# Kernel optimization log

Hardware: AMD Instinct MI355X
Metric: run time of the kernel (lower is better)

## Reference

```python
import jax, jax.numpy as jnp
import numpy as np

K = 20
EPS = 1e-5
NEG_SLOPE = 0.2


def _knn(x):
    # x: (B, C, N) -> idx of K nearest (largest negative sq dist): (B, N, K)
    inner = -2.0 * jnp.einsum('bcn,bcm->bnm', x, x)
    xx = jnp.sum(x * x, axis=1)  # (B, N)
    pd = -xx[:, :, None] - inner - xx[:, None, :]
    return jax.lax.top_k(pd, K)[1]


def _graph_feature(x):
    # x: (B, C, N) -> (B, 2C, N, K) edge features cat(nbr - center, center)
    idx = _knn(x)                              # (B, N, K)
    xt = jnp.swapaxes(x, 1, 2)                 # (B, N, C)
    nbr = jax.vmap(lambda f, i: f[i])(xt, idx)  # (B, N, K, C)
    center = xt[:, :, None, :]
    feat = jnp.concatenate([nbr - center, jnp.broadcast_to(center, nbr.shape)], axis=-1)
    return jnp.transpose(feat, (0, 3, 1, 2))


def _bn(x, g, b, m, v):
    # inference-mode batchnorm over channel axis 1
    shp = [1] * x.ndim
    shp[1] = -1
    scale = (g / jnp.sqrt(v + EPS)).reshape(shp)
    return (x - m.reshape(shp)) * scale + b.reshape(shp)


def _lrelu(x):
    return jnp.where(x >= 0, x, NEG_SLOPE * x)


def setup_inputs() -> dict:
    key = jax.random.key(0)
    ks = jax.random.split(key, 16)
    d = {
        'x': jax.random.normal(ks[0], (4, 2, 4096), jnp.float32),
        'W1': jax.random.normal(ks[1], (64, 4), jnp.float32),
        'g1': jax.random.uniform(ks[2], (64,), jnp.float32),
        'b1': jax.random.normal(ks[3], (64,), jnp.float32),
        'm1': jnp.zeros((64,), jnp.float32),
        'v1': jnp.ones((64,), jnp.float32),
        'W2': jax.random.normal(ks[4], (64, 128), jnp.float32),
        'g2': jax.random.uniform(ks[5], (64,), jnp.float32),
        'b2': jax.random.normal(ks[6], (64,), jnp.float32),
        'm2': jnp.zeros((64,), jnp.float32),
        'v2': jnp.ones((64,), jnp.float32),
        'W5': jax.random.normal(ks[7], (128, 128), jnp.float32),
        'g5': jax.random.uniform(ks[8], (128,), jnp.float32),
        'b5': jax.random.normal(ks[9], (128,), jnp.float32),
        'm5': jnp.zeros((128,), jnp.float32),
        'v5': jnp.ones((128,), jnp.float32),
        'W6': jax.random.normal(ks[10], (256, 256), jnp.float32),
        'g6': jax.random.uniform(ks[11], (256,), jnp.float32),
        'b6': jax.random.normal(ks[12], (256,), jnp.float32),
        'm6': jnp.zeros((256,), jnp.float32),
        'v6': jnp.ones((256,), jnp.float32),
        'W9': jax.random.normal(ks[13], (1, 256), jnp.float32),
    }
    return d


def reference(x, W1, g1, b1, m1, v1, W2, g2, b2, m2, v2,
              W5, g5, b5, m5, v5, W6, g6, b6, m6, v6, W9):
    B, _, N = x.shape
    # EdgeConv 1
    f = _graph_feature(x)                                     # (B, 4, N, K)
    h = _lrelu(_bn(jnp.einsum('bcnk,oc->bonk', f, W1), g1, b1, m1, v1))
    x1 = jnp.max(h, axis=-1)                                  # (B, 64, N)
    # EdgeConv 2 (graph rebuilt in feature space)
    f = _graph_feature(x1)                                    # (B, 128, N, K)
    h = _lrelu(_bn(jnp.einsum('bcnk,oc->bonk', f, W2), g2, b2, m2, v2))
    x2 = jnp.max(h, axis=-1)                                  # (B, 64, N)
    xc = jnp.concatenate([x1, x2], axis=1)                    # (B, 128, N)
    # conv5 (1x1 conv1d) + global max pool
    h5 = _lrelu(_bn(jnp.einsum('bcn,oc->bon', xc, W5), g5, b5, m5, v5))  # (B, 128, N)
    gmax = jnp.max(h5, axis=-1)                               # (B, 128)
    rep = jnp.broadcast_to(gmax[:, :, None], (B, gmax.shape[1], N))
    cat = jnp.concatenate([rep, xc], axis=1)                  # (B, 256, N)
    # conv6 (dropout is identity in eval) then conv9
    h6 = _lrelu(_bn(jnp.einsum('bcn,oc->bon', cat, W6), g6, b6, m6, v6))
    out = jnp.einsum('bcn,oc->bon', h6, W9)                   # (B, 1, N)
    return out.reshape(B, N)
```

## Files before the change

kernel.cpp:

```cpp
#include <hip/hip_runtime.h>
#include <math.h>

#define NEGINF (-INFINITY)
constexpr int Np = 4096;
constexpr int Kn = 20;
constexpr float EPSf = 1e-5f;
constexpr float SLOPE = 0.2f;

typedef __bf16 bf16x8 __attribute__((ext_vector_type(8)));
typedef float f32x4 __attribute__((ext_vector_type(4)));
typedef unsigned long long ull;
typedef unsigned int u32;
typedef unsigned short u16;

__global__ __launch_bounds__(512, 2) void k1_knn1_edge1(
    const float* __restrict__ x, const float* __restrict__ W1,
    const float* __restrict__ g1, const float* __restrict__ b1,
    const float* __restrict__ m1, const float* __restrict__ v1,
    float* __restrict__ x1, __bf16* __restrict__ x1h, __bf16* __restrict__ x1l,
    float* __restrict__ xx2)
{
  __shared__ u32 smem32[16000];
  float* pk1  = (float*)smem32;
  u16*   pi1  = (u16*)((char*)smem32 + 32768);
  u32*   thrK = (u32*)((char*)smem32 + 49152);
  u32*   ku   = smem32;
  u16*   ki   = (u16*)((char*)smem32 + 40960);
  u16*   midx = (u16*)((char*)smem32 + 61440);
  float* nbr  = (float*)smem32;

  const int b = blockIdx.y;
  const int n0 = blockIdx.x * 64;
  const int tid = threadIdx.x;
  const int w = tid >> 6, L = tid & 63;
  const float* __restrict__ xr = x + (size_t)b*2*Np;
  const float* __restrict__ yr = xr + Np;

  const int n = n0 + L;
  const float px = xr[n], py = yr[n];

  if (tid < 64) thrK[tid] = 0xFFFFFFFFu;
  __syncthreads();

  ull kv[20];
#pragma unroll
  for (int s = 0; s < 20; ++s) kv[s] = 0ull;
  u32 u_cut = 0xFFFFFFFFu;
  int cnt = 0;

  auto flushK = [&]() {
#pragma unroll 1
    for (int f0 = 0; f0 < 16; f0 += 4) {
      if (__all(f0 >= cnt)) break;
      float fv[4]; u32 ji[4];
#pragma unroll
      for (int u = 0; u < 4; ++u) {
        fv[u] = pk1[(f0+u)*512 + tid];
        ji[u] = pi1[(f0+u)*512 + tid];
      }
#pragma unroll
      for (int u = 0; u < 4; ++u) {
        int f = f0 + u;
        ull key = (((ull)(~__float_as_uint(fv[u]))) << 32) | (u32)~ji[u];
        if (f < cnt && key > kv[19]) {
          ull ck = key;
#pragma unroll
          for (int s = 0; s < 20; ++s) {
            bool sw = ck > kv[s];
            ull tv = kv[s];
            kv[s] = sw ? ck : kv[s];
            ck = sw ? tv : ck;
          }
        }
      }
    }
    cnt = 0;
    u32 uc = ~(u32)(kv[19] >> 32);
    atomicMin(&thrK[L], uc);
    u_cut = thrK[L];
  };

  const int base = w * 512;
#pragma unroll 1
  for (int j0 = base; j0 < base + 512; j0 += 16) {
    {
      u32 hs = thrK[L];
      u_cut = hs < u_cut ? hs : u_cut;
    }
#pragma unroll
    for (int c = 0; c < 4; ++c) {
      float4 xv = *reinterpret_cast<const float4*>(xr + j0 + c*4);
      float4 yv = *reinterpret_cast<const float4*>(yr + j0 + c*4);
      const float xs[4] = {xv.x, xv.y, xv.z, xv.w};
      const float ys[4] = {yv.x, yv.y, yv.z, yv.w};
#pragma unroll
      for (int r = 0; r < 4; ++r) {
        float dx = xs[r] - px, dy = ys[r] - py;
        float s = dx*dx + dy*dy;
        u32 ub = __float_as_uint(s);
        if (ub <= u_cut) {
          pk1[cnt*512 + tid] = s;
          pi1[cnt*512 + tid] = (u16)(j0 + c*4 + r);
          ++cnt;
        }
      }
      if (__any(cnt >= 13)) flushK();
    }
  }
  flushK();

  __syncthreads();
#pragma unroll
  for (int k = 0; k < Kn; ++k) {
    ku[((size_t)w*64 + L)*20 + k] = (u32)(kv[k] >> 32);
    ki[((size_t)w*64 + L)*20 + k] = (u16)~(u32)kv[k];
  }
  __syncthreads();

  if (tid < 64) {
    const int p = tid;
    u32 hk_[8]; u16 hj_[8]; int pc[8];
#pragma unroll
    for (int q = 0; q < 8; ++q) {
      size_t bi = ((size_t)q*64 + p)*20;
      hk_[q] = ku[bi]; hj_[q] = ki[bi]; pc[q] = 0;
    }
    for (int k = 0; k < Kn; ++k) {
      u32 bk = hk_[0]; u16 bj = hj_[0]; int sel = 0;
#pragma unroll
      for (int q = 1; q < 8; ++q) {
        bool better = (hk_[q] > bk) || (hk_[q] == bk && hj_[q] < bj);
        if (better) { bk = hk_[q]; bj = hj_[q]; sel = q; }
      }
      midx[p*20 + k] = bj;
      int np_ = ++pc[sel];
      size_t bi = ((size_t)sel*64 + p)*20;
      hk_[sel] = (np_ < 20) ? ku[bi + np_] : 0u;
      hj_[sel] = (np_ < 20) ? ki[bi + np_] : (u16)0xFFFF;
    }
  }
  __syncthreads();

  for (int i = tid; i < 64*Kn; i += 512) {
    int j = midx[i];
    nbr[i*2]     = xr[j];
    nbr[i*2 + 1] = yr[j];
  }
  __syncthreads();

  const int o = L;
  const float4 w1v = reinterpret_cast<const float4*>(W1)[o];
  const float sc = g1[o] / sqrtf(v1[o] + EPSf);
  const float mo = m1[o], bo = b1[o];

  for (int pi = 0; pi < 8; ++pi) {
    const int p = w*8 + pi;
    const int np = n0 + p;
    const float cx0 = xr[np], cx1 = yr[np];
    const float cterm = (w1v.z - w1v.x)*cx0 + (w1v.w - w1v.y)*cx1;
    float xm = NEGINF;
#pragma unroll
    for (int k = 0; k < Kn; ++k) {
      float2 nv = *reinterpret_cast<const float2*>(&nbr[(p*20 + k)*2]);
      float vv = w1v.x*nv.x + w1v.y*nv.y + cterm;
      float h = (vv - mo)*sc + bo;
      h = h >= 0.f ? h : SLOPE*h;
      xm = fmaxf(xm, h);
    }
    x1[(b*64 + o)*Np + np] = xm;
    __bf16 hb = (__bf16)xm;
    __bf16 lb = (__bf16)(xm - (float)hb);
    size_t tbase = ((size_t)b*Np + np)*64 + o;
    x1h[tbase] = hb;
    x1l[tbase] = lb;
    float s = xm*xm;
#pragma unroll
    for (int off = 1; off < 64; off <<= 1) s += __shfl_xor(s, off);
    if (L == 0) xx2[b*Np + np] = s;
  }
}

__global__ __launch_bounds__(256, 2) void k2_knn2(
    const __bf16* __restrict__ xh, const __bf16* __restrict__ xl,
    const float* __restrict__ xx2, int* __restrict__ idx2)
{
  __shared__ ull smem[5120];
  float* sxx = (float*)smem;
  float* pk  = (float*)((char*)smem + 16384);
  u16*   pi  = (u16*)((char*)smem + 31744);
  u32*   thr = (u32*)((char*)smem + 39424);

  const int b = blockIdx.y;
  const int n0 = blockIdx.x * 16;
  const int tid = threadIdx.x;
  const int w = tid >> 6, L = tid & 63;
  const int L15 = L & 15, quad = L >> 4;

  for (int j = tid*4; j < Np; j += 1024)
    *reinterpret_cast<float4*>(&sxx[j]) = *reinterpret_cast<const float4*>(&xx2[(size_t)b*Np + j]);
  if (tid < 16) thr[tid] = 0u;

  const __bf16* Rh = xh + ((size_t)b*Np + n0)*64;
  const __bf16* Rl = xl + ((size_t)b*Np + n0)*64;
  bf16x8 rh0 = *reinterpret_cast<const bf16x8*>(Rh + L15*64 +  0 + quad*8);
  bf16x8 rh1 = *reinterpret_cast<const bf16x8*>(Rh + L15*64 + 32 + quad*8);
  bf16x8 rl0 = *reinterpret_cast<const bf16x8*>(Rl + L15*64 +  0 + quad*8);
  bf16x8 rl1 = *reinterpret_cast<const bf16x8*>(Rl + L15*64 + 32 + quad*8);

  const __bf16* Cbh = xh + (size_t)b*Np*64;
  const __bf16* Cbl = xl + (size_t)b*Np*64;

  ull kv[20];
#pragma unroll
  for (int s = 0; s < 20; ++s) kv[s] = 0ull;
  float fthresh = NEGINF;
  int cnt = 0;

  __syncthreads();

  auto flush = [&]() {
#pragma unroll 1
    for (int f0 = 0; f0 < 15; f0 += 4) {
      if (__all(f0 >= cnt)) break;
      float fv[4]; u32 ji[4];
#pragma unroll
      for (int u = 0; u < 4; ++u) {
        fv[u] = pk[(f0+u)*256 + tid];
        ji[u] = pi[(f0+u)*256 + tid];
      }
#pragma unroll
      for (int u = 0; u < 4; ++u) {
        int f = f0 + u;
        u32 uu = __float_as_uint(fv[u]);
        u32 hk = uu ^ ((u32)((int)uu >> 31) | 0x80000000u);
        ull key = (((ull)hk) << 32) | (u32)~ji[u];
        if (f < cnt && key > kv[19]) {
          ull ck = key;
#pragma unroll
          for (int s = 0; s < 20; ++s) {
            bool sw = ck > kv[s];
            ull tv = kv[s];
            kv[s] = sw ? ck : kv[s];
            ck = sw ? tv : ck;
          }
        }
      }
    }
    cnt = 0;
    ull t = kv[19];
    ull t2 = __shfl_xor(t, 16); t = t2 > t ? t2 : t;
    t2 = __shfl_xor(t, 32);     t = t2 > t ? t2 : t;
    if (t != 0ull && quad == 0) atomicMax(&thr[L15], (u32)(t >> 32));
    u32 hs = thr[L15];
    if (hs != 0u) {
      u32 u = (hs >> 31) ? (hs ^ 0x80000000u) : ~hs;
      fthresh = fmaxf(fthresh, __uint_as_float(u));
    }
  };

#pragma unroll 1
  for (int t = 0; t < 16; ++t) {
    {
      u32 hs = thr[L15];
      if (hs != 0u) {
        u32 u = (hs >> 31) ? (hs ^ 0x80000000u) : ~hs;
        fthresh = fmaxf(fthresh, __uint_as_float(u));
      }
    }
    const int tt = w + t*4;
    const int colbase = tt * 64;
    const __bf16* ph = Cbh + (size_t)colbase*64;
    const __bf16* pl = Cbl + (size_t)colbase*64;
    bf16x8 AH[4][2], AL[4][2];
#pragma unroll
    for (int s = 0; s < 4; ++s) {
      AH[s][0] = *reinterpret_cast<const bf16x8*>(ph + (s*16 + L15)*64 +  0 + quad*8);
      AH[s][1] = *reinterpret_cast<const bf16x8*>(ph + (s*16 + L15)*64 + 32 + quad*8);
      AL[s][0] = *reinterpret_cast<const bf16x8*>(pl + (s*16 + L15)*64 +  0 + quad*8);
      AL[s][1] = *reinterpret_cast<const bf16x8*>(pl + (s*16 + L15)*64 + 32 + quad*8);
    }

    f32x4 acc[4];
#pragma unroll
    for (int s = 0; s < 4; ++s) {
      acc[s] = (f32x4){0.f, 0.f, 0.f, 0.f};
      acc[s] = __builtin_amdgcn_mfma_f32_16x16x32_bf16(AH[s][0], rh0, acc[s], 0, 0, 0);
      acc[s] = __builtin_amdgcn_mfma_f32_16x16x32_bf16(AH[s][1], rh1, acc[s], 0, 0, 0);
      acc[s] = __builtin_amdgcn_mfma_f32_16x16x32_bf16(AH[s][0], rl0, acc[s], 0, 0, 0);
      acc[s] = __builtin_amdgcn_mfma_f32_16x16x32_bf16(AH[s][1], rl1, acc[s], 0, 0, 0);
      acc[s] = __builtin_amdgcn_mfma_f32_16x16x32_bf16(AL[s][0], rh0, acc[s], 0, 0, 0);
      acc[s] = __builtin_amdgcn_mfma_f32_16x16x32_bf16(AL[s][1], rh1, acc[s], 0, 0, 0);
    }

#pragma unroll
    for (int s = 0; s < 4; ++s) {
      float4 xv = *reinterpret_cast<const float4*>(&sxx[colbase + s*16 + quad*4]);
      const float xvr[4] = {xv.x, xv.y, xv.z, xv.w};
#pragma unroll
      for (int r = 0; r < 4; ++r) {
        float e = 2.0f*acc[s][r] - xvr[r];
        if (e >= fthresh) {
          pk[cnt*256 + tid] = e;
          pi[cnt*256 + tid] = (u16)(colbase + s*16 + quad*4 + r);
          ++cnt;
        }
      }
      if (__any(cnt >= 12)) flush();
    }
  }
  flush();

  __syncthreads();
#pragma unroll
  for (int k = 0; k < Kn; ++k) smem[((size_t)w*64 + L)*20 + k] = kv[k];
  __syncthreads();

  if (tid < 16) {
    const int r = tid;
    ull h[16]; int pc[16];
#pragma unroll
    for (int i = 0; i < 16; ++i) {
      h[i] = smem[((size_t)(i>>2)*64 + (i&3)*16 + r)*20];
      pc[i] = 0;
    }
    size_t obase = ((size_t)b*Np + n0 + r)*Kn;
    for (int k = 0; k < Kn; ++k) {
      ull best = h[0]; int sel = 0;
#pragma unroll
      for (int i = 1; i < 16; ++i) if (h[i] > best) { best = h[i]; sel = i; }
      idx2[obase + k] = (int)~(u32)best;
      int np_ = ++pc[sel];
      h[sel] = (np_ < 20) ? smem[((size_t)(sel>>2)*64 + (sel&3)*16 + r)*20 + np_] : 0ull;
    }
  }
}

__global__ __launch_bounds__(256) void kY(
    const __bf16* __restrict__ xh, const __bf16* __restrict__ xl,
    const float* __restrict__ W2,
    const float* __restrict__ g2, const float* __restrict__ b2,
    const float* __restrict__ m2, const float* __restrict__ v2,
    float* __restrict__ Za, float* __restrict__ Cn)
{
  __shared__ float w2t[128*66];
  const int b = blockIdx.y;
  const int n0 = blockIdx.x * 16;
  const int tid = threadIdx.x;
  const int w = tid >> 6, L = tid & 63;

  for (int i = tid; i < 8192; i += 256) {
    int o = i >> 7, c = i & 127;
    w2t[c*66 + o] = W2[i];
  }
  __syncthreads();

  const float sc = g2[L] / sqrtf(v2[L] + EPSf);
  const float cc = b2[L] - m2[L]*sc;

  for (int pi = 0; pi < 4; ++pi) {
    const int n = n0 + w*4 + pi;
    const size_t base = ((size_t)b*Np + n)*64;
    const float xv = (float)xh[base + L] + (float)xl[base + L];
    float ya = 0.f, yb = 0.f;
#pragma unroll
    for (int c = 0; c < 64; ++c) {
      float xc = __shfl(xv, c);
      ya += w2t[c*66 + L] * xc;
      yb += w2t[(64 + c)*66 + L] * xc;
    }
    float za = sc * ya;
    Za[base + L] = za;
    Cn[base + L] = sc * yb + cc - za;
  }
}

__global__ __launch_bounds__(256, 2) void k3_gather(
    const float* __restrict__ Za, const float* __restrict__ Cn,
    const int* __restrict__ idx2, float* __restrict__ x2)
{
  const int b = blockIdx.y;
  const int tid = threadIdx.x;
  const int w = tid >> 6, L = tid & 63;
  const int n = blockIdx.x*4 + w;

  const int* ip = idx2 + ((size_t)b*Np + n)*Kn;
  int jreg = (L < Kn) ? ip[L] : 0;
  const float c = Cn[((size_t)b*Np + n)*64 + L];
  float xm = NEGINF;
#pragma unroll
  for (int k = 0; k < Kn; ++k) {
    int j = __shfl(jreg, k);
    float hh = Za[((size_t)b*Np + j)*64 + L] + c;
    hh = hh >= 0.f ? hh : SLOPE*hh;
    xm = fmaxf(xm, hh);
  }
  x2[(b*64 + L)*Np + n] = xm;
}

__global__ __launch_bounds__(512) void k4_conv5max(
    const float* __restrict__ x1, const float* __restrict__ x2,
    const float* __restrict__ W5,
    const float* __restrict__ g5, const float* __restrict__ b5,
    const float* __restrict__ m5, const float* __restrict__ v5,
    float* __restrict__ partials)
{
  const int b = blockIdx.y;
  const int nb = blockIdx.x >> 1, half = blockIdx.x & 1;
  const int tid = threadIdx.x;
  const int p = tid & 63;
  const int g = __builtin_amdgcn_readfirstlane(tid >> 6);
  const int n = nb*64 + p;
  float xcr[128];
#pragma unroll
  for (int c = 0; c < 64; ++c) {
    xcr[c]    = x1[(b*64 + c)*Np + n];
    xcr[64+c] = x2[(b*64 + c)*Np + n];
  }
  for (int oi = 0; oi < 8; ++oi) {
    const int o = half*64 + g*8 + oi;
    const float* wr = W5 + o*128;
    float dot = 0.f;
#pragma unroll
    for (int c = 0; c < 128; c += 4) {
      float4 wv = *reinterpret_cast<const float4*>(wr + c);
      dot += wv.x*xcr[c] + wv.y*xcr[c+1] + wv.z*xcr[c+2] + wv.w*xcr[c+3];
    }
    float hv = (dot - m5[o])*(g5[o]/sqrtf(v5[o]+EPSf)) + b5[o];
    hv = hv >= 0.f ? hv : SLOPE*hv;
#pragma unroll
    for (int off = 1; off < 64; off <<= 1) hv = fmaxf(hv, __shfl_xor(hv, off));
    if (p == 0) partials[(b*128 + o)*64 + nb] = hv;
  }
}

__global__ __launch_bounds__(256) void k5_reduce_t6(
    const float* __restrict__ partials, const float* __restrict__ W6,
    float* __restrict__ t6)
{
  __shared__ float sg[128];
  const int b = blockIdx.x;
  const int tid = threadIdx.x;
  if (tid < 128) {
    const float4* pr = reinterpret_cast<const float4*>(partials + ((size_t)b*128 + tid)*64);
    float m = NEGINF;
#pragma unroll
    for (int w = 0; w < 16; ++w) {
      float4 v = pr[w];
      m = fmaxf(m, fmaxf(fmaxf(v.x, v.y), fmaxf(v.z, v.w)));
    }
    sg[tid] = m;
  }
  __syncthreads();
  float a = 0.f;
#pragma unroll
  for (int c = 0; c < 128; c += 4) {
    float4 wv = *reinterpret_cast<const float4*>(W6 + tid*256 + c);
    a += wv.x*sg[c] + wv.y*sg[c+1] + wv.z*sg[c+2] + wv.w*sg[c+3];
  }
  t6[b*256 + tid] = a;
}

__global__ __launch_bounds__(512) void k6_conv6_out(
    const float* __restrict__ x1, const float* __restrict__ x2,
    const float* __restrict__ W6, const float* __restrict__ t6,
    const float* __restrict__ g6, const float* __restrict__ b6,
    const float* __restrict__ m6, const float* __restrict__ v6,
    const float* __restrict__ W9,
    float* __restrict__ out)
{
  __shared__ float red[8][64];
  const int b = blockIdx.y, nb = blockIdx.x;
  const int tid = threadIdx.x;
  const int p = tid & 63;
  const int g = __builtin_amdgcn_readfirstlane(tid >> 6);
  const int n = nb*64 + p;
  float xcr[128];
#pragma unroll
  for (int c = 0; c < 64; ++c) {
    xcr[c]    = x1[(b*64 + c)*Np + n];
    xcr[64+c] = x2[(b*64 + c)*Np + n];
  }
  float oacc = 0.f;
  for (int oi = 0; oi < 32; ++oi) {
    const int o = g*32 + oi;
    const float* wr = W6 + o*256 + 128;
    float dot = t6[b*256 + o];
#pragma unroll
    for (int c = 0; c < 128; c += 4) {
      float4 wv = *reinterpret_cast<const float4*>(wr + c);
      dot += wv.x*xcr[c] + wv.y*xcr[c+1] + wv.z*xcr[c+2] + wv.w*xcr[c+3];
    }
    float hv = (dot - m6[o])*(g6[o]/sqrtf(v6[o]+EPSf)) + b6[o];
    hv = hv >= 0.f ? hv : SLOPE*hv;
    oacc += W9[o]*hv;
  }
  red[g][p] = oacc;
  __syncthreads();
  if (tid < 64) {
    float s = 0.f;
#pragma unroll
    for (int q = 0; q < 8; ++q) s += red[q][tid];
    out[b*Np + nb*64 + tid] = s;
  }
}

extern "C" void kernel_launch(void* const* d_in, const int* in_sizes, int n_in,
                              void* d_out, int out_size, void* d_ws, size_t ws_size,
                              hipStream_t stream) {
  const float* x  = (const float*)d_in[0];
  const float* W1 = (const float*)d_in[1];
  const float* g1 = (const float*)d_in[2];
  const float* b1 = (const float*)d_in[3];
  const float* m1 = (const float*)d_in[4];
  const float* v1 = (const float*)d_in[5];
  const float* W2 = (const float*)d_in[6];
  const float* g2 = (const float*)d_in[7];
  const float* b2 = (const float*)d_in[8];
  const float* m2 = (const float*)d_in[9];
  const float* v2 = (const float*)d_in[10];
  const float* W5 = (const float*)d_in[11];
  const float* g5 = (const float*)d_in[12];
  const float* b5 = (const float*)d_in[13];
  const float* m5 = (const float*)d_in[14];
  const float* v5 = (const float*)d_in[15];
  const float* W6 = (const float*)d_in[16];
  const float* g6 = (const float*)d_in[17];
  const float* b6 = (const float*)d_in[18];
  const float* m6 = (const float*)d_in[19];
  const float* v6 = (const float*)d_in[20];
  const float* W9 = (const float*)d_in[21];
  float* out = (float*)d_out;

  float* F = (float*)d_ws;
  float*  x1    = F;
  float*  xx2   = F + 1048576;
  __bf16* x1h   = (__bf16*)(F + 1064960);
  __bf16* x1l   = (__bf16*)(F + 1589248);
  float*  x2    = F + 2113536;
  int*    idx2  = (int*)(F + 3162112);
  float*  t6    = F + 3489792;
  float*  parts = F + 3490816;
  float*  Za    = F + 3523584;
  float*  Cn    = F + 4572160;

  k1_knn1_edge1<<<dim3(64,4), 512, 0, stream>>>(x, W1, g1, b1, m1, v1, x1, x1h, x1l, xx2);
  k2_knn2<<<dim3(256,4), 256, 0, stream>>>(x1h, x1l, xx2, idx2);
  kY<<<dim3(256,4), 256, 0, stream>>>(x1h, x1l, W2, g2, b2, m2, v2, Za, Cn);
  k3_gather<<<dim3(1024,4), 256, 0, stream>>>(Za, Cn, idx2, x2);
  k4_conv5max<<<dim3(128,4), 512, 0, stream>>>(x1, x2, W5, g5, b5, m5, v5, parts);
  k5_reduce_t6<<<4, 256, 0, stream>>>(parts, W6, t6);
  k6_conv6_out<<<dim3(64,4), 512, 0, stream>>>(x1, x2, W6, t6, g6, b6, m6, v6, W9, out);
}
```

Measured before the change: 524.9 us.

## Fuse W2 projection into knn1 kernel and split conv6 output channels across blocks

The per-point W2 projection (Za/Cn) is moved from a separate kernel into the tail of the first EdgeConv kernel. It reuses the freshly computed x1 values held in registers, which avoids a launch and a reread of x1h/x1l. Separately, conv6 is split across twice as many blocks, each covering half the output channels, with partial results combined by atomicAdd into an output zeroed by a memset. This adds LDS use and tail work to k1, which runs only 256 blocks, plus an extra memset and atomics. It also changes the float summation order, and the fused path now reads exact fp32 x1 instead of the bf16 hi+lo reconstruction.

```diff
diff --git a/kernel.cpp b/kernel.cpp
--- a/kernel.cpp
+++ b/kernel.cpp
@@ -17,8 +17,11 @@
     const float* __restrict__ x, const float* __restrict__ W1,
     const float* __restrict__ g1, const float* __restrict__ b1,
     const float* __restrict__ m1, const float* __restrict__ v1,
+    const float* __restrict__ W2,
+    const float* __restrict__ g2, const float* __restrict__ b2,
+    const float* __restrict__ m2, const float* __restrict__ v2,
     float* __restrict__ x1, __bf16* __restrict__ x1h, __bf16* __restrict__ x1l,
-    float* __restrict__ xx2)
+    float* __restrict__ xx2, float* __restrict__ Za, float* __restrict__ Cn)
 {
   __shared__ u32 smem32[16000];
   float* pk1  = (float*)smem32;
@@ -28,6 +31,7 @@
   u16*   ki   = (u16*)((char*)smem32 + 40960);
   u16*   midx = (u16*)((char*)smem32 + 61440);
   float* nbr  = (float*)smem32;
+  float* w2t  = (float*)((char*)smem32 + 12288);
 
   const int b = blockIdx.y;
   const int n0 = blockIdx.x * 64;
@@ -146,12 +150,18 @@
     nbr[i*2]     = xr[j];
     nbr[i*2 + 1] = yr[j];
   }
+  for (int i = tid; i < 8192; i += 512) {
+    int o = i >> 7, c = i & 127;
+    w2t[c*66 + o] = W2[i];
+  }
   __syncthreads();
 
   const int o = L;
   const float4 w1v = reinterpret_cast<const float4*>(W1)[o];
   const float sc = g1[o] / sqrtf(v1[o] + EPSf);
   const float mo = m1[o], bo = b1[o];
+  const float sc2 = g2[o] / sqrtf(v2[o] + EPSf);
+  const float cc2 = b2[o] - m2[o]*sc2;
 
   for (int pi = 0; pi < 8; ++pi) {
     const int p = w*8 + pi;
@@ -177,6 +187,17 @@
 #pragma unroll
     for (int off = 1; off < 64; off <<= 1) s += __shfl_xor(s, off);
     if (L == 0) xx2[b*Np + np] = s;
+
+    float ya = 0.f, yb = 0.f;
+#pragma unroll
+    for (int c = 0; c < 64; ++c) {
+      float xc = __shfl(xm, c);
+      ya += w2t[c*66 + o] * xc;
+      yb += w2t[(64 + c)*66 + o] * xc;
+    }
+    float za = sc2 * ya;
+    Za[tbase] = za;
+    Cn[tbase] = sc2 * yb + cc2 - za;
   }
 }
 
@@ -332,45 +353,6 @@
       int np_ = ++pc[sel];
       h[sel] = (np_ < 20) ? smem[((size_t)(sel>>2)*64 + (sel&3)*16 + r)*20 + np_] : 0ull;
     }
-  }
-}
-
-__global__ __launch_bounds__(256) void kY(
-    const __bf16* __restrict__ xh, const __bf16* __restrict__ xl,
-    const float* __restrict__ W2,
-    const float* __restrict__ g2, const float* __restrict__ b2,
-    const float* __restrict__ m2, const float* __restrict__ v2,
-    float* __restrict__ Za, float* __restrict__ Cn)
-{
-  __shared__ float w2t[128*66];
-  const int b = blockIdx.y;
-  const int n0 = blockIdx.x * 16;
-  const int tid = threadIdx.x;
-  const int w = tid >> 6, L = tid & 63;
-
-  for (int i = tid; i < 8192; i += 256) {
-    int o = i >> 7, c = i & 127;
-    w2t[c*66 + o] = W2[i];
-  }
-  __syncthreads();
-
-  const float sc = g2[L] / sqrtf(v2[L] + EPSf);
-  const float cc = b2[L] - m2[L]*sc;
-
-  for (int pi = 0; pi < 4; ++pi) {
-    const int n = n0 + w*4 + pi;
-    const size_t base = ((size_t)b*Np + n)*64;
-    const float xv = (float)xh[base + L] + (float)xl[base + L];
-    float ya = 0.f, yb = 0.f;
-#pragma unroll
-    for (int c = 0; c < 64; ++c) {
-      float xc = __shfl(xv, c);
-      ya += w2t[c*66 + L] * xc;
-      yb += w2t[(64 + c)*66 + L] * xc;
-    }
-    float za = sc * ya;
-    Za[base + L] = za;
-    Cn[base + L] = sc * yb + cc - za;
   }
 }
 
@@ -469,7 +451,8 @@
     float* __restrict__ out)
 {
   __shared__ float red[8][64];
-  const int b = blockIdx.y, nb = blockIdx.x;
+  const int b = blockIdx.y;
+  const int nb = blockIdx.x >> 1, half = blockIdx.x & 1;
   const int tid = threadIdx.x;
   const int p = tid & 63;
   const int g = __builtin_amdgcn_readfirstlane(tid >> 6);
@@ -481,8 +464,8 @@
     xcr[64+c] = x2[(b*64 + c)*Np + n];
   }
   float oacc = 0.f;
-  for (int oi = 0; oi < 32; ++oi) {
-    const int o = g*32 + oi;
+  for (int oi = 0; oi < 16; ++oi) {
+    const int o = half*128 + g*16 + oi;
     const float* wr = W6 + o*256 + 128;
     float dot = t6[b*256 + o];
 #pragma unroll
@@ -500,7 +483,7 @@
     float s = 0.f;
 #pragma unroll
     for (int q = 0; q < 8; ++q) s += red[q][tid];
-    out[b*Np + nb*64 + tid] = s;
+    atomicAdd(&out[b*Np + nb*64 + tid], s);
   }
 }
 
@@ -543,11 +526,13 @@
   float*  Za    = F + 3523584;
   float*  Cn    = F + 4572160;
 
-  k1_knn1_edge1<<<dim3(64,4), 512, 0, stream>>>(x, W1, g1, b1, m1, v1, x1, x1h, x1l, xx2);
+  k1_knn1_edge1<<<dim3(64,4), 512, 0, stream>>>(x, W1, g1, b1, m1, v1,
+                                                W2, g2, b2, m2, v2,
+                                                x1, x1h, x1l, xx2, Za, Cn);
   k2_knn2<<<dim3(256,4), 256, 0, stream>>>(x1h, x1l, xx2, idx2);
-  kY<<<dim3(256,4), 256, 0, stream>>>(x1h, x1l, W2, g2, b2, m2, v2, Za, Cn);
   k3_gather<<<dim3(1024,4), 256, 0, stream>>>(Za, Cn, idx2, x2);
   k4_conv5max<<<dim3(128,4), 512, 0, stream>>>(x1, x2, W5, g5, b5, m5, v5, parts);
   k5_reduce_t6<<<4, 256, 0, stream>>>(parts, W6, t6);
-  k6_conv6_out<<<dim3(64,4), 512, 0, stream>>>(x1, x2, W6, t6, g6, b6, m6, v6, W9, out);
-}
+  hipMemsetAsync(out, 0, out_size, stream);
+  k6_conv6_out<<<dim3(128,4), 512, 0, stream>>>(x1, x2, W6, t6, g6, b6, m6, v6, W9, out);
+}
```

Result: no change. 530.9 us (median of 2 runs) (+1.1%).
